# Kernel tuning notes

Hardware: AMD Instinct MI355X
Metric: run time of the kernel (lower is better)

Reference implementation:

```python
import jax, jax.numpy as jnp
import numpy as np

N_NODES = 100000


def setup_inputs() -> dict:
    key = jax.random.key(0)
    k1, k2, k3 = jax.random.split(key, 3)
    x = jax.random.normal(k1, (N_NODES, 256), dtype=jnp.float32)
    edge_index = jax.random.randint(k2, (2, 1600000), 0, N_NODES, dtype=jnp.int64)
    W = jax.random.normal(k3, (256, 128), dtype=jnp.float32) * (1.0 / np.sqrt(256.0))
    b = jnp.zeros((128,), dtype=jnp.float32)
    alpha = jnp.full((128,), 0.25, dtype=jnp.float32)  # PReLU default init
    return {"x": x, "edge_index": edge_index, "W": W, "b": b, "alpha": alpha}


def reference(x, edge_index, W, b, alpha):
    N = x.shape[0]
    # --- GCNConv: add self-loops ---
    loops = jnp.arange(N, dtype=edge_index.dtype)
    row = jnp.concatenate([edge_index[0], loops])  # source nodes
    col = jnp.concatenate([edge_index[1], loops])  # destination nodes
    # symmetric normalization: deg computed at destinations (self-loops => deg >= 1)
    deg = jax.ops.segment_sum(jnp.ones(col.shape, x.dtype), col, num_segments=N)
    dinv = jax.lax.rsqrt(deg)
    norm = dinv[row] * dinv[col]  # [E+N]
    # linear transform then normalized scatter-add aggregation
    h = x @ W  # [N, H]
    msg = h[row] * norm[:, None]  # [E+N, H]
    out = jax.ops.segment_sum(msg, col, num_segments=N) + b  # bias after aggregation
    # --- PReLU (per-channel) ---
    return jnp.where(out >= 0, out, alpha * out)
```

## Files before the change

### kernel.cpp

```cpp
#include <hip/hip_runtime.h>

constexpr int KDIM  = 256;
constexpr int HDIM  = 128;
constexpr int BK    = 128;
constexpr int CHUNK = 8192;
constexpr int NBMAX = 800;

typedef __bf16 bf16x8 __attribute__((ext_vector_type(8)));
typedef float  f32x4  __attribute__((ext_vector_type(4)));

__device__ __forceinline__ ushort f2bf(float f) {
    unsigned u = __float_as_uint(f);
    unsigned r = (u + 0x7fffu + ((u >> 16) & 1u)) >> 16;
    return (ushort)r;
}

__device__ __forceinline__ void accum8(float* a, uint4 u) {
    a[0] += __uint_as_float(u.x << 16); a[1] += __uint_as_float(u.x & 0xffff0000u);
    a[2] += __uint_as_float(u.y << 16); a[3] += __uint_as_float(u.y & 0xffff0000u);
    a[4] += __uint_as_float(u.z << 16); a[5] += __uint_as_float(u.z & 0xffff0000u);
    a[6] += __uint_as_float(u.w << 16); a[7] += __uint_as_float(u.w & 0xffff0000u);
}

__global__ __launch_bounds__(512) void prep_sort_kernel(
    const float* __restrict__ W, ushort* __restrict__ Wt, ushort* __restrict__ hsb,
    const int* __restrict__ row, const int* __restrict__ col,
    uint* __restrict__ ebuf, int* __restrict__ histG, int* __restrict__ localOff,
    int n, int e, int nbv, int gblk) {
    __shared__ uint dst[CHUNK];
    __shared__ int hist[NBMAX], excl[NBMAX], cur[NBMAX];
    __shared__ int ws2[8];
    int b = blockIdx.x, t = threadIdx.x;
    if (b < 8) {
        int g = b * 512 + t;
        int lane = g & 63, cn = g >> 6;
        int c = cn >> 3, nf = cn & 7;
        int ncol = nf * 16 + (lane & 15);
        int k0 = c * 32 + (lane >> 4) * 8;
        ushort* dp = Wt + (size_t)g * 8;
        #pragma unroll
        for (int j = 0; j < 8; ++j) dp[j] = f2bf(W[(k0 + j) * HDIM + ncol]);
        return;
    }
    if (b == 8) {
        if (t < HDIM) hsb[(size_t)n * HDIM + t] = 0;
        return;
    }
    int g = b - 9;
    int lane = t & 63, w = t >> 6;
    for (int i = t; i < nbv; i += 512) hist[i] = 0;
    __syncthreads();
    int lo = g * CHUNK, hi = min(lo + CHUNK, e);
    int colr[16];
    #pragma unroll
    for (int k = 0; k < 4; ++k) {
        int i0 = lo + (k * 512 + t) * 4;
        if (i0 + 3 < hi) {
            int4 c4 = *(const int4*)(col + i0);
            colr[k * 4 + 0] = c4.x; colr[k * 4 + 1] = c4.y;
            colr[k * 4 + 2] = c4.z; colr[k * 4 + 3] = c4.w;
            atomicAdd(&hist[c4.x >> 7], 1); atomicAdd(&hist[c4.y >> 7], 1);
            atomicAdd(&hist[c4.z >> 7], 1); atomicAdd(&hist[c4.w >> 7], 1);
        } else {
            #pragma unroll
            for (int j = 0; j < 4; ++j) {
                int i = i0 + j;
                int c = (i < hi) ? col[i] : -1;
                colr[k * 4 + j] = c;
                if (c >= 0) atomicAdd(&hist[c >> 7], 1);
            }
        }
    }
    __syncthreads();
    {
        int b0 = t * 2;
        int h0 = (b0 < nbv) ? hist[b0] : 0;
        int h1 = (b0 + 1 < nbv) ? hist[b0 + 1] : 0;
        int s = h0 + h1, incl = s;
        #pragma unroll
        for (int d = 1; d < 64; d <<= 1) { int u = __shfl_up(incl, d, 64); if (lane >= d) incl += u; }
        if (lane == 63) ws2[w] = incl;
        __syncthreads();
        int add = 0;
        #pragma unroll
        for (int i = 0; i < 8; ++i) if (i < w) add += ws2[i];
        int run = add + incl - s;
        if (b0 < nbv)     { excl[b0] = run;          cur[b0] = run; }
        if (b0 + 1 < nbv) { excl[b0 + 1] = run + h0; cur[b0 + 1] = run + h0; }
    }
    __syncthreads();
    #pragma unroll
    for (int k = 0; k < 4; ++k) {
        int i0 = lo + (k * 512 + t) * 4;
        if (i0 + 3 < hi) {
            int4 r4 = *(const int4*)(row + i0);
            int rr[4] = {r4.x, r4.y, r4.z, r4.w};
            #pragma unroll
            for (int j = 0; j < 4; ++j) {
                int c = colr[k * 4 + j];
                int p = atomicAdd(&cur[c >> 7], 1);
                dst[p] = ((uint)rr[j] << 7) | (uint)(c & 127);
            }
        } else {
            #pragma unroll
            for (int j = 0; j < 4; ++j) {
                int i = i0 + j, c = colr[k * 4 + j];
                if (c >= 0) {
                    int p = atomicAdd(&cur[c >> 7], 1);
                    dst[p] = ((uint)row[i] << 7) | (uint)(c & 127);
                }
            }
        }
    }
    __syncthreads();
    int cnt = hi - lo;
    for (int k = 0; k < 4; ++k) {
        int i0 = (k * 512 + t) * 4;
        if (i0 + 3 < cnt) *(uint4*)(ebuf + lo + i0) = *(uint4*)&dst[i0];
        else for (int j = 0; j < 4; ++j) if (i0 + j < cnt) ebuf[lo + i0 + j] = dst[i0 + j];
    }
    for (int i = t; i < nbv; i += 512) {
        histG[i * gblk + g]    = hist[i];
        localOff[i * gblk + g] = excl[i];
    }
}

__global__ __launch_bounds__(256) void scanA_kernel(const int* __restrict__ in,
                                                    int* __restrict__ partial, int n) {
    int t = threadIdx.x, base = blockIdx.x * 1024;
    int s = 0;
    #pragma unroll
    for (int j = 0; j < 4; ++j) {
        int i = base + j * 256 + t;
        if (i < n) s += in[i];
    }
    __shared__ int ws[4];
    #pragma unroll
    for (int d = 1; d < 64; d <<= 1) s += __shfl_xor(s, d, 64);
    int lane = t & 63, w = t >> 6;
    if (lane == 0) ws[w] = s;
    __syncthreads();
    if (t == 0) partial[blockIdx.x] = ws[0] + ws[1] + ws[2] + ws[3];
}

__global__ void scanB_kernel(int* __restrict__ partial, int nb) {
    int t = threadIdx.x;
    int v = (t < nb) ? partial[t] : 0;
    int orig = v;
    int lane = t & 63, w = t >> 6;
    #pragma unroll
    for (int d = 1; d < 64; d <<= 1) { int u = __shfl_up(v, d, 64); if (lane >= d) v += u; }
    __shared__ int ws[4];
    if (lane == 63) ws[w] = v;
    __syncthreads();
    int add = 0;
    #pragma unroll
    for (int i = 0; i < 4; ++i) if (i < w) add += ws[i];
    if (t < nb) partial[t] = v + add - orig;
}

__global__ __launch_bounds__(256) void scanC_kernel(const int* __restrict__ in,
                                                    const int* __restrict__ partial,
                                                    int* __restrict__ out, int n) {
    int t = threadIdx.x, base = blockIdx.x * 1024;
    int vals[4], tsum = 0;
    #pragma unroll
    for (int j = 0; j < 4; ++j) {
        int i = base + t * 4 + j;
        vals[j] = (i < n) ? in[i] : 0;
        tsum += vals[j];
    }
    int lane = t & 63, w = t >> 6;
    int incl = tsum;
    #pragma unroll
    for (int d = 1; d < 64; d <<= 1) { int u = __shfl_up(incl, d, 64); if (lane >= d) incl += u; }
    __shared__ int ws[4];
    if (lane == 63) ws[w] = incl;
    __syncthreads();
    int add = partial[blockIdx.x];
    #pragma unroll
    for (int i = 0; i < 4; ++i) if (i < w) add += ws[i];
    int run = add + incl - tsum;
    #pragma unroll
    for (int j = 0; j < 4; ++j) {
        int i = base + t * 4 + j;
        if (i < n) out[i] = run;
        run += vals[j];
    }
}

__global__ __launch_bounds__(256) void fine_kernel(const uint* __restrict__ ebuf,
                                                   const int* __restrict__ histG,
                                                   const int* __restrict__ localOff,
                                                   const int* __restrict__ histS,
                                                   uint* __restrict__ csr,
                                                   int* __restrict__ deg,
                                                   int* __restrict__ offs,
                                                   float* __restrict__ dinv,
                                                   int e, int nbv, int gblk, int n) {
    __shared__ uint elist[4096];
    __shared__ uint csrl[4096];
    __shared__ int hist[BK], excl[BK], cur[BK];
    int b = blockIdx.x, t = threadIdx.x;
    int seg0 = histS[b * gblk];
    int seg1 = (b + 1 < nbv) ? histS[(b + 1) * gblk] : e;
    int cnt = min(seg1 - seg0, 4096);

    if (t < BK) { hist[t] = 0; cur[t] = 0; }
    for (int g = t; g < gblk; g += 256) {
        int c   = histG[b * gblk + g];
        int src = g * CHUNK + localOff[b * gblk + g];
        int dst = histS[b * gblk + g] - seg0;
        for (int i = 0; i < c; ++i) elist[dst + i] = ebuf[src + i];
    }
    __syncthreads();
    for (int i = t; i < cnt; i += 256) atomicAdd(&hist[elist[i] & 127], 1);
    __syncthreads();
    if (t < 64) {
        int v0 = hist[2 * t], v1 = hist[2 * t + 1];
        int s = v0 + v1, incl = s;
        #pragma unroll
        for (int d = 1; d < 64; d <<= 1) { int u = __shfl_up(incl, d, 64); if (t >= d) incl += u; }
        int base = incl - s;
        excl[2 * t] = base; excl[2 * t + 1] = base + v0;
    }
    __syncthreads();
    for (int i = t; i < cnt; i += 256) {
        uint v = elist[i];
        int d = v & 127;
        int r = atomicAdd(&cur[d], 1);
        csrl[excl[d] + r] = v >> 7;
    }
    __syncthreads();
    for (int i = t; i < cnt; i += 256) csr[seg0 + i] = csrl[i];
    if (t < BK) {
        int node = b * BK + t;
        if (node < n) {
            int dg = hist[t];
            deg[node]  = dg;
            offs[node] = seg0 + excl[t];
            dinv[node] = rsqrtf((float)(dg + 1));
        }
    }
}


constexpr int MT = 64;
constexpr int XS_STRIDE = 264;

__global__ __launch_bounds__(256) void gemm_kernel(const float* __restrict__ x,
                                                   const ushort* __restrict__ Wt,
                                                   const float* __restrict__ dinv,
                                                   ushort* __restrict__ hsb, int n) {
    __shared__ ushort xs[MT * XS_STRIDE];
    __shared__ float sdinv[MT];
    int t = threadIdx.x, lane = t & 63, w = t >> 6;
    int row0 = blockIdx.x * MT;

    bf16x8 bfrag[8][2];
    #pragma unroll
    for (int c = 0; c < 8; ++c)
        #pragma unroll
        for (int f = 0; f < 2; ++f)
            bfrag[c][f] = *(const bf16x8*)(Wt + (size_t)(((c * 8) + (w * 2 + f)) * 64 + lane) * 8);

    #pragma unroll
    for (int i = 0; i < 16; ++i) {
        int rl = w * 16 + i;
        int gr = row0 + rl; if (gr >= n) gr = n - 1;
        float4 v = *(const float4*)(x + (size_t)gr * KDIM + lane * 4);
        ushort4 o;
        o.x = f2bf(v.x); o.y = f2bf(v.y); o.z = f2bf(v.z); o.w = f2bf(v.w);
        *(ushort4*)(xs + rl * XS_STRIDE + lane * 4) = o;
    }
    if (t < MT) { int g = row0 + t; sdinv[t] = dinv[(g < n) ? g : (n - 1)]; }
    __syncthreads();

    #pragma unroll
    for (int s = 0; s < MT / 16; ++s) {
        f32x4 acc0 = {0.f, 0.f, 0.f, 0.f}, acc1 = {0.f, 0.f, 0.f, 0.f};
        #pragma unroll
        for (int c = 0; c < 8; ++c) {
            const ushort* ap = xs + (s * 16 + (lane & 15)) * XS_STRIDE + c * 32 + (lane >> 4) * 8;
            bf16x8 afrag = *(const bf16x8*)ap;
            acc0 = __builtin_amdgcn_mfma_f32_16x16x32_bf16(afrag, bfrag[c][0], acc0, 0, 0, 0);
            acc1 = __builtin_amdgcn_mfma_f32_16x16x32_bf16(afrag, bfrag[c][1], acc1, 0, 0, 0);
        }
        #pragma unroll
        for (int reg = 0; reg < 4; ++reg) {
            int rl = s * 16 + (lane >> 4) * 4 + reg;
            int gr = row0 + rl;
            if (gr < n) {
                float d = sdinv[rl];
                int col0 = w * 32 + (lane & 15);
                hsb[(size_t)gr * HDIM + col0]      = f2bf(acc0[reg] * d);
                hsb[(size_t)gr * HDIM + col0 + 16] = f2bf(acc1[reg] * d);
            }
        }
    }
}


__global__ __launch_bounds__(256) void aggregate_kernel(
    const ushort* __restrict__ hsb, const int* __restrict__ offs,
    const int* __restrict__ deg, const int* __restrict__ csr,
    const float* __restrict__ dinv, const float* __restrict__ b,
    const float* __restrict__ alpha, float* __restrict__ out, int n) {
    int wv = threadIdx.x >> 6, lane = threadIdx.x & 63;
    int grp = lane >> 4, li = lane & 15;
    int node = blockIdx.x * 16 + wv * 4 + grp;
    bool valid = node < n;
    int nd   = valid ? node : n;
    int base = valid ? offs[node] : 0;
    int cnt  = valid ? deg[node] : 0;
    const uint4* hs4 = (const uint4*)hsb;

    float a[8];
    #pragma unroll
    for (int i = 0; i < 8; ++i) a[i] = 0.f;

    uint4 su = hs4[(size_t)nd * 16 + li];
    accum8(a, su);

    for (int it = 0; it < cnt; it += 16) {
        int src_l = (it + li < cnt) ? (int)__builtin_nontemporal_load(csr + base + it + li) : n;

        int sA[8];
        #pragma unroll
        for (int k = 0; k < 8; ++k) sA[k] = __shfl(src_l, grp * 16 + k, 64);
        uint4 uA[8];
        #pragma unroll
        for (int k = 0; k < 8; ++k) uA[k] = hs4[(size_t)sA[k] * 16 + li];
        #pragma unroll
        for (int k = 0; k < 8; ++k) accum8(a, uA[k]);

        if (it + 8 < cnt) {
            int sB[8];
            #pragma unroll
            for (int k = 0; k < 8; ++k) sB[k] = __shfl(src_l, grp * 16 + 8 + k, 64);
            uint4 uB[8];
            #pragma unroll
            for (int k = 0; k < 8; ++k) uB[k] = hs4[(size_t)sB[k] * 16 + li];
            #pragma unroll
            for (int k = 0; k < 8; ++k) accum8(a, uB[k]);
        }
    }

    if (valid) {
        float dc = dinv[node];
        int c0 = li * 8;
        float o[8];
        #pragma unroll
        for (int i = 0; i < 8; ++i) {
            float v = fmaf(dc, a[i], b[c0 + i]);
            o[i] = v >= 0.f ? v : alpha[c0 + i] * v;
        }
        float* op = out + (size_t)node * HDIM + c0;
        f32x4 v0 = {o[0], o[1], o[2], o[3]};
        f32x4 v1 = {o[4], o[5], o[6], o[7]};
        __builtin_nontemporal_store(v0, (f32x4*)op);
        __builtin_nontemporal_store(v1, (f32x4*)(op + 4));
    }
}


extern "C" void kernel_launch(void* const* d_in, const int* in_sizes, int n_in,
                              void* d_out, int out_size, void* d_ws, size_t ws_size,
                              hipStream_t stream) {
    const float* x     = (const float*)d_in[0];
    const int*   ei    = (const int*)d_in[1];
    const float* W     = (const float*)d_in[2];
    const float* b     = (const float*)d_in[3];
    const float* alpha = (const float*)d_in[4];
    float* out = (float*)d_out;

    int E = in_sizes[1] / 2;
    int N = in_sizes[0] / KDIM;
    int NB = (N + BK - 1) / BK;
    int GBLK = (E + CHUNK - 1) / CHUNK;
    int SCAN_N = NB * GBLK;

    ushort* hsb   = (ushort*)d_ws;
    ushort* Wt    = hsb + (size_t)(N + 1) * HDIM;
    float* dinv   = (float*)(Wt + 32768);
    int* deg      = (int*)(dinv + N);
    int* offs     = deg + N;
    int* histG    = offs + N;
    int* localOff = histG + SCAN_N;
    int* histS    = localOff + SCAN_N;
    int* partial  = histS + SCAN_N;
    uint* ebuf    = (uint*)(partial + 512);
    uint* csr     = ebuf + (size_t)GBLK * CHUNK;

    const int* rowp = ei;
    const int* colp = ei + E;

    int nbScan = (SCAN_N + 1023) / 1024;

    hipLaunchKernelGGL(prep_sort_kernel, dim3(9 + GBLK), dim3(512), 0, stream,
                       W, Wt, hsb, rowp, colp, ebuf, histG, localOff, N, E, NB, GBLK);
    hipLaunchKernelGGL(scanA_kernel, dim3(nbScan), dim3(256), 0, stream, histG, partial, SCAN_N);
    hipLaunchKernelGGL(scanB_kernel, dim3(1), dim3(256), 0, stream, partial, nbScan);
    hipLaunchKernelGGL(scanC_kernel, dim3(nbScan), dim3(256), 0, stream, histG, partial, histS, SCAN_N);
    hipLaunchKernelGGL(fine_kernel, dim3(NB), dim3(256), 0, stream,
                       ebuf, histG, localOff, histS, csr, deg, offs, dinv, E, NB, GBLK, N);
    hipLaunchKernelGGL(gemm_kernel, dim3((N + MT - 1) / MT), dim3(256), 0, stream, x, Wt, dinv, hsb, N);
    hipLaunchKernelGGL(aggregate_kernel, dim3((N + 15) / 16), dim3(256), 0, stream,
                       hsb, offs, deg, (const int*)csr, dinv, b, alpha, out, N);
}
```

Before: 294.3 us.

## Replace two-level bucket sort CSR build with global-atomic counting sort

Replaces the LDS-based two-pass bucketed sort (chunk histograms, a scan over bucket×chunk, then a per-bucket fine sort) with a direct counting sort. Per-node degree comes from global atomics, a scan over N yields offsets and dinv, and a scatter pass places row ids with global atomicAdd on per-node cursors. This removes the intermediate ebuf and fine_kernel passes, at the cost of heavy global atomic traffic and randomly ordered writes into the CSR. Neighbor order within each node becomes nondeterministic.

Measured after the change: 417.3 us. 1.42x slower.

```diff
diff --git a/kernel.cpp b/kernel.cpp
--- a/kernel.cpp
+++ b/kernel.cpp
@@ -2,9 +2,7 @@
 
 constexpr int KDIM  = 256;
 constexpr int HDIM  = 128;
-constexpr int BK    = 128;
 constexpr int CHUNK = 8192;
-constexpr int NBMAX = 800;
 
 typedef __bf16 bf16x8 __attribute__((ext_vector_type(8)));
 typedef float  f32x4  __attribute__((ext_vector_type(4)));
@@ -22,14 +20,9 @@
     a[6] += __uint_as_float(u.w << 16); a[7] += __uint_as_float(u.w & 0xffff0000u);
 }
 
-__global__ __launch_bounds__(512) void prep_sort_kernel(
+__global__ __launch_bounds__(512) void prep_hist_kernel(
     const float* __restrict__ W, ushort* __restrict__ Wt, ushort* __restrict__ hsb,
-    const int* __restrict__ row, const int* __restrict__ col,
-    uint* __restrict__ ebuf, int* __restrict__ histG, int* __restrict__ localOff,
-    int n, int e, int nbv, int gblk) {
-    __shared__ uint dst[CHUNK];
-    __shared__ int hist[NBMAX], excl[NBMAX], cur[NBMAX];
-    __shared__ int ws2[8];
+    const int* __restrict__ col, int* __restrict__ deg, int n, int e) {
     int b = blockIdx.x, t = threadIdx.x;
     if (b < 8) {
         int g = b * 512 + t;
@@ -47,81 +40,20 @@
         return;
     }
     int g = b - 9;
-    int lane = t & 63, w = t >> 6;
-    for (int i = t; i < nbv; i += 512) hist[i] = 0;
-    __syncthreads();
     int lo = g * CHUNK, hi = min(lo + CHUNK, e);
-    int colr[16];
     #pragma unroll
     for (int k = 0; k < 4; ++k) {
         int i0 = lo + (k * 512 + t) * 4;
         if (i0 + 3 < hi) {
             int4 c4 = *(const int4*)(col + i0);
-            colr[k * 4 + 0] = c4.x; colr[k * 4 + 1] = c4.y;
-            colr[k * 4 + 2] = c4.z; colr[k * 4 + 3] = c4.w;
-            atomicAdd(&hist[c4.x >> 7], 1); atomicAdd(&hist[c4.y >> 7], 1);
-            atomicAdd(&hist[c4.z >> 7], 1); atomicAdd(&hist[c4.w >> 7], 1);
+            atomicAdd(&deg[c4.x], 1); atomicAdd(&deg[c4.y], 1);
+            atomicAdd(&deg[c4.z], 1); atomicAdd(&deg[c4.w], 1);
         } else {
-            #pragma unroll
             for (int j = 0; j < 4; ++j) {
                 int i = i0 + j;
-                int c = (i < hi) ? col[i] : -1;
-                colr[k * 4 + j] = c;
-                if (c >= 0) atomicAdd(&hist[c >> 7], 1);
+                if (i < hi) atomicAdd(&deg[col[i]], 1);
             }
         }
-    }
-    __syncthreads();
-    {
-        int b0 = t * 2;
-        int h0 = (b0 < nbv) ? hist[b0] : 0;
-        int h1 = (b0 + 1 < nbv) ? hist[b0 + 1] : 0;
-        int s = h0 + h1, incl = s;
-        #pragma unroll
-        for (int d = 1; d < 64; d <<= 1) { int u = __shfl_up(incl, d, 64); if (lane >= d) incl += u; }
-        if (lane == 63) ws2[w] = incl;
-        __syncthreads();
-        int add = 0;
-        #pragma unroll
-        for (int i = 0; i < 8; ++i) if (i < w) add += ws2[i];
-        int run = add + incl - s;
-        if (b0 < nbv)     { excl[b0] = run;          cur[b0] = run; }
-        if (b0 + 1 < nbv) { excl[b0 + 1] = run + h0; cur[b0 + 1] = run + h0; }
-    }
-    __syncthreads();
-    #pragma unroll
-    for (int k = 0; k < 4; ++k) {
-        int i0 = lo + (k * 512 + t) * 4;
-        if (i0 + 3 < hi) {
-            int4 r4 = *(const int4*)(row + i0);
-            int rr[4] = {r4.x, r4.y, r4.z, r4.w};
-            #pragma unroll
-            for (int j = 0; j < 4; ++j) {
-                int c = colr[k * 4 + j];
-                int p = atomicAdd(&cur[c >> 7], 1);
-                dst[p] = ((uint)rr[j] << 7) | (uint)(c & 127);
-            }
-        } else {
-            #pragma unroll
-            for (int j = 0; j < 4; ++j) {
-                int i = i0 + j, c = colr[k * 4 + j];
-                if (c >= 0) {
-                    int p = atomicAdd(&cur[c >> 7], 1);
-                    dst[p] = ((uint)row[i] << 7) | (uint)(c & 127);
-                }
-            }
-        }
-    }
-    __syncthreads();
-    int cnt = hi - lo;
-    for (int k = 0; k < 4; ++k) {
-        int i0 = (k * 512 + t) * 4;
-        if (i0 + 3 < cnt) *(uint4*)(ebuf + lo + i0) = *(uint4*)&dst[i0];
-        else for (int j = 0; j < 4; ++j) if (i0 + j < cnt) ebuf[lo + i0 + j] = dst[i0 + j];
-    }
-    for (int i = t; i < nbv; i += 512) {
-        histG[i * gblk + g]    = hist[i];
-        localOff[i * gblk + g] = excl[i];
     }
 }
 
@@ -159,15 +91,17 @@
     if (t < nb) partial[t] = v + add - orig;
 }
 
-__global__ __launch_bounds__(256) void scanC_kernel(const int* __restrict__ in,
-                                                    const int* __restrict__ partial,
-                                                    int* __restrict__ out, int n) {
+__global__ __launch_bounds__(256) void scanC2_kernel(const int* __restrict__ deg,
+                                                     const int* __restrict__ partial,
+                                                     int* __restrict__ offs,
+                                                     int* __restrict__ cur,
+                                                     float* __restrict__ dinv, int n) {
     int t = threadIdx.x, base = blockIdx.x * 1024;
     int vals[4], tsum = 0;
     #pragma unroll
     for (int j = 0; j < 4; ++j) {
         int i = base + t * 4 + j;
-        vals[j] = (i < n) ? in[i] : 0;
+        vals[j] = (i < n) ? deg[i] : 0;
         tsum += vals[j];
     }
     int lane = t & 63, w = t >> 6;
@@ -184,62 +118,41 @@
     #pragma unroll
     for (int j = 0; j < 4; ++j) {
         int i = base + t * 4 + j;
-        if (i < n) out[i] = run;
+        if (i < n) {
+            offs[i] = run;
+            cur[i]  = run;
+            dinv[i] = rsqrtf((float)(vals[j] + 1));
+        }
         run += vals[j];
     }
 }
 
-__global__ __launch_bounds__(256) void fine_kernel(const uint* __restrict__ ebuf,
-                                                   const int* __restrict__ histG,
-                                                   const int* __restrict__ localOff,
-                                                   const int* __restrict__ histS,
-                                                   uint* __restrict__ csr,
-                                                   int* __restrict__ deg,
-                                                   int* __restrict__ offs,
-                                                   float* __restrict__ dinv,
-                                                   int e, int nbv, int gblk, int n) {
-    __shared__ uint elist[4096];
-    __shared__ uint csrl[4096];
-    __shared__ int hist[BK], excl[BK], cur[BK];
-    int b = blockIdx.x, t = threadIdx.x;
-    int seg0 = histS[b * gblk];
-    int seg1 = (b + 1 < nbv) ? histS[(b + 1) * gblk] : e;
-    int cnt = min(seg1 - seg0, 4096);
-
-    if (t < BK) { hist[t] = 0; cur[t] = 0; }
-    for (int g = t; g < gblk; g += 256) {
-        int c   = histG[b * gblk + g];
-        int src = g * CHUNK + localOff[b * gblk + g];
-        int dst = histS[b * gblk + g] - seg0;
-        for (int i = 0; i < c; ++i) elist[dst + i] = ebuf[src + i];
-    }
-    __syncthreads();
-    for (int i = t; i < cnt; i += 256) atomicAdd(&hist[elist[i] & 127], 1);
-    __syncthreads();
-    if (t < 64) {
-        int v0 = hist[2 * t], v1 = hist[2 * t + 1];
-        int s = v0 + v1, incl = s;
-        #pragma unroll
-        for (int d = 1; d < 64; d <<= 1) { int u = __shfl_up(incl, d, 64); if (t >= d) incl += u; }
-        int base = incl - s;
-        excl[2 * t] = base; excl[2 * t + 1] = base + v0;
-    }
-    __syncthreads();
-    for (int i = t; i < cnt; i += 256) {
-        uint v = elist[i];
-        int d = v & 127;
-        int r = atomicAdd(&cur[d], 1);
-        csrl[excl[d] + r] = v >> 7;
-    }
-    __syncthreads();
-    for (int i = t; i < cnt; i += 256) csr[seg0 + i] = csrl[i];
-    if (t < BK) {
-        int node = b * BK + t;
-        if (node < n) {
-            int dg = hist[t];
-            deg[node]  = dg;
-            offs[node] = seg0 + excl[t];
-            dinv[node] = rsqrtf((float)(dg + 1));
+__global__ __launch_bounds__(512) void scatter_kernel(const int* __restrict__ row,
+                                                      const int* __restrict__ col,
+                                                      int* __restrict__ cur,
+                                                      uint* __restrict__ csr, int e) {
+    int t = threadIdx.x;
+    int lo = blockIdx.x * CHUNK, hi = min(lo + CHUNK, e);
+    #pragma unroll
+    for (int k = 0; k < 4; ++k) {
+        int i0 = lo + (k * 512 + t) * 4;
+        if (i0 + 3 < hi) {
+            int4 c4 = *(const int4*)(col + i0);
+            int4 r4 = *(const int4*)(row + i0);
+            int p0 = atomicAdd(&cur[c4.x], 1);
+            int p1 = atomicAdd(&cur[c4.y], 1);
+            int p2 = atomicAdd(&cur[c4.z], 1);
+            int p3 = atomicAdd(&cur[c4.w], 1);
+            csr[p0] = (uint)r4.x; csr[p1] = (uint)r4.y;
+            csr[p2] = (uint)r4.z; csr[p3] = (uint)r4.w;
+        } else {
+            for (int j = 0; j < 4; ++j) {
+                int i = i0 + j;
+                if (i < hi) {
+                    int p = atomicAdd(&cur[col[i]], 1);
+                    csr[p] = (uint)row[i];
+                }
+            }
         }
     }
 }
@@ -300,10 +213,9 @@
     }
 }
 
-
 __global__ __launch_bounds__(256) void aggregate_kernel(
     const ushort* __restrict__ hsb, const int* __restrict__ offs,
-    const int* __restrict__ deg, const int* __restrict__ csr,
+    const int* __restrict__ deg, const uint* __restrict__ csr,
     const float* __restrict__ dinv, const float* __restrict__ b,
     const float* __restrict__ alpha, float* __restrict__ out, int n) {
     int wv = threadIdx.x >> 6, lane = threadIdx.x & 63;
@@ -376,35 +288,32 @@
 
     int E = in_sizes[1] / 2;
     int N = in_sizes[0] / KDIM;
-    int NB = (N + BK - 1) / BK;
     int GBLK = (E + CHUNK - 1) / CHUNK;
-    int SCAN_N = NB * GBLK;
 
     ushort* hsb   = (ushort*)d_ws;
     ushort* Wt    = hsb + (size_t)(N + 1) * HDIM;
     float* dinv   = (float*)(Wt + 32768);
     int* deg      = (int*)(dinv + N);
     int* offs     = deg + N;
-    int* histG    = offs + N;
-    int* localOff = histG + SCAN_N;
-    int* histS    = localOff + SCAN_N;
-    int* partial  = histS + SCAN_N;
-    uint* ebuf    = (uint*)(partial + 512);
-    uint* csr     = ebuf + (size_t)GBLK * CHUNK;
+    int* cur      = offs + N;
+    int* partial  = cur + N;
+    uint* csr     = (uint*)(partial + 512);
 
     const int* rowp = ei;
     const int* colp = ei + E;
 
-    int nbScan = (SCAN_N + 1023) / 1024;
-
-    hipLaunchKernelGGL(prep_sort_kernel, dim3(9 + GBLK), dim3(512), 0, stream,
-                       W, Wt, hsb, rowp, colp, ebuf, histG, localOff, N, E, NB, GBLK);
-    hipLaunchKernelGGL(scanA_kernel, dim3(nbScan), dim3(256), 0, stream, histG, partial, SCAN_N);
-    hipLaunchKernelGGL(scanB_kernel, dim3(1), dim3(256), 0, stream, partial, nbScan);
-    hipLaunchKernelGGL(scanC_kernel, dim3(nbScan), dim3(256), 0, stream, histG, partial, histS, SCAN_N);
-    hipLaunchKernelGGL(fine_kernel, dim3(NB), dim3(256), 0, stream,
-                       ebuf, histG, localOff, histS, csr, deg, offs, dinv, E, NB, GBLK, N);
+    int nbScanN = (N + 1023) / 1024;
+
+    hipMemsetAsync(deg, 0, (size_t)N * sizeof(int), stream);
+    hipLaunchKernelGGL(prep_hist_kernel, dim3(9 + GBLK), dim3(512), 0, stream,
+                       W, Wt, hsb, colp, deg, N, E);
+    hipLaunchKernelGGL(scanA_kernel, dim3(nbScanN), dim3(256), 0, stream, deg, partial, N);
+    hipLaunchKernelGGL(scanB_kernel, dim3(1), dim3(256), 0, stream, partial, nbScanN);
+    hipLaunchKernelGGL(scanC2_kernel, dim3(nbScanN), dim3(256), 0, stream,
+                       deg, partial, offs, cur, dinv, N);
+    hipLaunchKernelGGL(scatter_kernel, dim3(GBLK), dim3(512), 0, stream,
+                       rowp, colp, cur, csr, E);
     hipLaunchKernelGGL(gemm_kernel, dim3((N + MT - 1) / MT), dim3(256), 0, stream, x, Wt, dinv, hsb, N);
     hipLaunchKernelGGL(aggregate_kernel, dim3((N + 15) / 16), dim3(256), 0, stream,
-                       hsb, offs, deg, (const int*)csr, dinv, b, alpha, out, N);
-}
+                       hsb, offs, deg, csr, dinv, b, alpha, out, N);
+}
```

## Quantize intermediate node features to int8 with per-row scales for gather

Applied to the files above, without the earlier changes.

The GEMM epilogue now quantizes each scaled output row to int8 using a per-row absmax scale, computed through a shared-memory atomicMax. The aggregation kernel then gathers 8-byte int8 vectors plus one float scale per neighbour instead of 16-byte bf16 vectors. This halves the bytes of the random-access gather that dominates the kernel, at the cost of extra syncs in the GEMM, extra scale loads and reduced numerical precision.

New measurement: 281.5 us. 1.05x faster.

```diff
diff --git a/kernel.cpp b/kernel.cpp
--- a/kernel.cpp
+++ b/kernel.cpp
@@ -15,15 +15,21 @@
     return (ushort)r;
 }
 
-__device__ __forceinline__ void accum8(float* a, uint4 u) {
-    a[0] += __uint_as_float(u.x << 16); a[1] += __uint_as_float(u.x & 0xffff0000u);
-    a[2] += __uint_as_float(u.y << 16); a[3] += __uint_as_float(u.y & 0xffff0000u);
-    a[4] += __uint_as_float(u.z << 16); a[5] += __uint_as_float(u.z & 0xffff0000u);
-    a[6] += __uint_as_float(u.w << 16); a[7] += __uint_as_float(u.w & 0xffff0000u);
+__device__ __forceinline__ void acc8i(float* a, uint2 u, float s) {
+    int x = (int)u.x, y = (int)u.y;
+    a[0] += s * (float)((x << 24) >> 24);
+    a[1] += s * (float)((x << 16) >> 24);
+    a[2] += s * (float)((x <<  8) >> 24);
+    a[3] += s * (float)( x        >> 24);
+    a[4] += s * (float)((y << 24) >> 24);
+    a[5] += s * (float)((y << 16) >> 24);
+    a[6] += s * (float)((y <<  8) >> 24);
+    a[7] += s * (float)( y        >> 24);
 }
 
 __global__ __launch_bounds__(512) void prep_sort_kernel(
-    const float* __restrict__ W, ushort* __restrict__ Wt, ushort* __restrict__ hsb,
+    const float* __restrict__ W, ushort* __restrict__ Wt, char* __restrict__ hsb8,
+    float* __restrict__ hscale,
     const int* __restrict__ row, const int* __restrict__ col,
     uint* __restrict__ ebuf, int* __restrict__ histG, int* __restrict__ localOff,
     int n, int e, int nbv, int gblk) {
@@ -43,7 +49,8 @@
         return;
     }
     if (b == 8) {
-        if (t < HDIM) hsb[(size_t)n * HDIM + t] = 0;
+        if (t < 32) ((uint*)(hsb8 + (size_t)n * HDIM))[t] = 0;
+        if (t == 32) hscale[n] = 0.f;
         return;
     }
     int g = b - 9;
@@ -251,9 +258,11 @@
 __global__ __launch_bounds__(256) void gemm_kernel(const float* __restrict__ x,
                                                    const ushort* __restrict__ Wt,
                                                    const float* __restrict__ dinv,
-                                                   ushort* __restrict__ hsb, int n) {
+                                                   char* __restrict__ hsb8,
+                                                   float* __restrict__ hscale, int n) {
     __shared__ ushort xs[MT * XS_STRIDE];
     __shared__ float sdinv[MT];
+    __shared__ uint rmaxs[16];
     int t = threadIdx.x, lane = t & 63, w = t >> 6;
     int row0 = blockIdx.x * MT;
 
@@ -276,7 +285,6 @@
     if (t < MT) { int g = row0 + t; sdinv[t] = dinv[(g < n) ? g : (n - 1)]; }
     __syncthreads();
 
-    #pragma unroll
     for (int s = 0; s < MT / 16; ++s) {
         f32x4 acc0 = {0.f, 0.f, 0.f, 0.f}, acc1 = {0.f, 0.f, 0.f, 0.f};
         #pragma unroll
@@ -286,26 +294,50 @@
             acc0 = __builtin_amdgcn_mfma_f32_16x16x32_bf16(afrag, bfrag[c][0], acc0, 0, 0, 0);
             acc1 = __builtin_amdgcn_mfma_f32_16x16x32_bf16(afrag, bfrag[c][1], acc1, 0, 0, 0);
         }
+        if (t < 16) rmaxs[t] = 0;
+        __syncthreads();
+        float v0[4], v1[4];
         #pragma unroll
         for (int reg = 0; reg < 4; ++reg) {
             int rl = s * 16 + (lane >> 4) * 4 + reg;
             int gr = row0 + rl;
             if (gr < n) {
                 float d = sdinv[rl];
+                v0[reg] = acc0[reg] * d;
+                v1[reg] = acc1[reg] * d;
+                float m = fmaxf(fabsf(v0[reg]), fabsf(v1[reg]));
+                atomicMax(&rmaxs[(lane >> 4) * 4 + reg], __float_as_uint(m));
+            }
+        }
+        __syncthreads();
+        #pragma unroll
+        for (int reg = 0; reg < 4; ++reg) {
+            int rl = s * 16 + (lane >> 4) * 4 + reg;
+            int gr = row0 + rl;
+            if (gr < n) {
+                float rm = __uint_as_float(rmaxs[(lane >> 4) * 4 + reg]);
+                float inv = (rm > 0.f) ? 127.f / rm : 0.f;
+                int q0 = __float2int_rn(v0[reg] * inv);
+                int q1 = __float2int_rn(v1[reg] * inv);
                 int col0 = w * 32 + (lane & 15);
-                hsb[(size_t)gr * HDIM + col0]      = f2bf(acc0[reg] * d);
-                hsb[(size_t)gr * HDIM + col0 + 16] = f2bf(acc1[reg] * d);
+                hsb8[(size_t)gr * HDIM + col0]      = (char)q0;
+                hsb8[(size_t)gr * HDIM + col0 + 16] = (char)q1;
             }
         }
-    }
-}
-
+        if (t < 16) {
+            int gr = row0 + s * 16 + t;
+            if (gr < n) hscale[gr] = __uint_as_float(rmaxs[t]) * (1.f / 127.f);
+        }
+        __syncthreads();
+    }
+}
 
 __global__ __launch_bounds__(256) void aggregate_kernel(
-    const ushort* __restrict__ hsb, const int* __restrict__ offs,
-    const int* __restrict__ deg, const int* __restrict__ csr,
-    const float* __restrict__ dinv, const float* __restrict__ b,
-    const float* __restrict__ alpha, float* __restrict__ out, int n) {
+    const char* __restrict__ hsb8, const float* __restrict__ hscale,
+    const int* __restrict__ offs, const int* __restrict__ deg,
+    const uint* __restrict__ csr, const float* __restrict__ dinv,
+    const float* __restrict__ b, const float* __restrict__ alpha,
+    float* __restrict__ out, int n) {
     int wv = threadIdx.x >> 6, lane = threadIdx.x & 63;
     int grp = lane >> 4, li = lane & 15;
     int node = blockIdx.x * 16 + wv * 4 + grp;
@@ -313,14 +345,14 @@
     int nd   = valid ? node : n;
     int base = valid ? offs[node] : 0;
     int cnt  = valid ? deg[node] : 0;
-    const uint4* hs4 = (const uint4*)hsb;
+    const uint2* hs2 = (const uint2*)hsb8;
 
     float a[8];
     #pragma unroll
     for (int i = 0; i < 8; ++i) a[i] = 0.f;
 
-    uint4 su = hs4[(size_t)nd * 16 + li];
-    accum8(a, su);
+    uint2 su = hs2[(size_t)nd * 16 + li];
+    acc8i(a, su, hscale[nd]);
 
     for (int it = 0; it < cnt; it += 16) {
         int src_l = (it + li < cnt) ? (int)__builtin_nontemporal_load(csr + base + it + li) : n;
@@ -328,21 +360,27 @@
         int sA[8];
         #pragma unroll
         for (int k = 0; k < 8; ++k) sA[k] = __shfl(src_l, grp * 16 + k, 64);
-        uint4 uA[8];
-        #pragma unroll
-        for (int k = 0; k < 8; ++k) uA[k] = hs4[(size_t)sA[k] * 16 + li];
-        #pragma unroll
-        for (int k = 0; k < 8; ++k) accum8(a, uA[k]);
+        uint2 uA[8];
+        float scA[8];
+        #pragma unroll
+        for (int k = 0; k < 8; ++k) uA[k] = hs2[(size_t)sA[k] * 16 + li];
+        #pragma unroll
+        for (int k = 0; k < 8; ++k) scA[k] = hscale[sA[k]];
+        #pragma unroll
+        for (int k = 0; k < 8; ++k) acc8i(a, uA[k], scA[k]);
 
         if (it + 8 < cnt) {
             int sB[8];
             #pragma unroll
             for (int k = 0; k < 8; ++k) sB[k] = __shfl(src_l, grp * 16 + 8 + k, 64);
-            uint4 uB[8];
-            #pragma unroll
-            for (int k = 0; k < 8; ++k) uB[k] = hs4[(size_t)sB[k] * 16 + li];
-            #pragma unroll
-            for (int k = 0; k < 8; ++k) accum8(a, uB[k]);
+            uint2 uB[8];
+            float scB[8];
+            #pragma unroll
+            for (int k = 0; k < 8; ++k) uB[k] = hs2[(size_t)sB[k] * 16 + li];
+            #pragma unroll
+            for (int k = 0; k < 8; ++k) scB[k] = hscale[sB[k]];
+            #pragma unroll
+            for (int k = 0; k < 8; ++k) acc8i(a, uB[k], scB[k]);
         }
     }
 
@@ -380,8 +418,9 @@
     int GBLK = (E + CHUNK - 1) / CHUNK;
     int SCAN_N = NB * GBLK;
 
-    ushort* hsb   = (ushort*)d_ws;
-    ushort* Wt    = hsb + (size_t)(N + 1) * HDIM;
+    char*  hsb8   = (char*)d_ws;
+    float* hscale = (float*)(hsb8 + (size_t)(N + 1) * HDIM);
+    ushort* Wt    = (ushort*)(hscale + (N + 1));
     float* dinv   = (float*)(Wt + 32768);
     int* deg      = (int*)(dinv + N);
     int* offs     = deg + N;
@@ -398,13 +437,14 @@
     int nbScan = (SCAN_N + 1023) / 1024;
 
     hipLaunchKernelGGL(prep_sort_kernel, dim3(9 + GBLK), dim3(512), 0, stream,
-                       W, Wt, hsb, rowp, colp, ebuf, histG, localOff, N, E, NB, GBLK);
+                       W, Wt, hsb8, hscale, rowp, colp, ebuf, histG, localOff, N, E, NB, GBLK);
     hipLaunchKernelGGL(scanA_kernel, dim3(nbScan), dim3(256), 0, stream, histG, partial, SCAN_N);
     hipLaunchKernelGGL(scanB_kernel, dim3(1), dim3(256), 0, stream, partial, nbScan);
     hipLaunchKernelGGL(scanC_kernel, dim3(nbScan), dim3(256), 0, stream, histG, partial, histS, SCAN_N);
     hipLaunchKernelGGL(fine_kernel, dim3(NB), dim3(256), 0, stream,
                        ebuf, histG, localOff, histS, csr, deg, offs, dinv, E, NB, GBLK, N);
-    hipLaunchKernelGGL(gemm_kernel, dim3((N + MT - 1) / MT), dim3(256), 0, stream, x, Wt, dinv, hsb, N);
+    hipLaunchKernelGGL(gemm_kernel, dim3((N + MT - 1) / MT), dim3(256), 0, stream,
+                       x, Wt, dinv, hsb8, hscale, N);
     hipLaunchKernelGGL(aggregate_kernel, dim3((N + 15) / 16), dim3(256), 0, stream,
-                       hsb, offs, deg, (const int*)csr, dinv, b, alpha, out, N);
-}
+                       hsb8, hscale, offs, deg, csr, dinv, b, alpha, out, N);
+}
```
